# Kernel optimization log

Hardware: AMD Instinct MI355X
Metric: run time of the kernel (lower is better)

## Reference

```python
import jax, jax.numpy as jnp
import numpy as np

INPUT_H = 512
INPUT_W = 512
POOL = 5
BN_EPS = 1e-5


def setup_inputs() -> dict:
    key = jax.random.key(0)
    ks = jax.random.split(key, 8)
    B = 16
    c3 = jax.random.normal(ks[0], (B, 512, 64, 64), jnp.float32)
    c4 = jax.random.normal(ks[1], (B, 1024, 32, 32), jnp.float32)
    xy = jax.random.uniform(ks[2], (B, 10, 4), jnp.float32) * 512.0
    # ensure x1<=x2, y1<=y2 like real detector boxes
    boxes = jnp.concatenate([jnp.minimum(xy[..., :2], xy[..., 2:]),
                             jnp.maximum(xy[..., :2], xy[..., 2:])], axis=-1)
    w_conv = jax.random.normal(ks[3], (512, 1536), jnp.float32) * 0.02  # 1x1 conv kernel
    b_conv = jnp.zeros((512,), jnp.float32)
    bn_gamma = jnp.ones((512,), jnp.float32)
    bn_beta = jnp.zeros((512,), jnp.float32)
    bn_mean = jax.random.normal(ks[4], (512,), jnp.float32) * 0.1
    bn_var = jax.random.uniform(ks[5], (512,), jnp.float32) * 0.5 + 0.5
    return {"c3": c3, "c4": c4, "boxes": boxes, "w_conv": w_conv, "b_conv": b_conv,
            "bn_gamma": bn_gamma, "bn_beta": bn_beta, "bn_mean": bn_mean, "bn_var": bn_var}


def _bin_weights(lo, hi, size, nout):
    """Adaptive-avg-pool bin weights over axis of length `size` for crop [lo,hi).
    Returns [nout, size] row-stochastic matrix (same math as AdaptiveAvgPool1d bins)."""
    length = hi - lo
    k = jnp.arange(nout)
    starts = lo + (k * length) // nout                      # floor(k*L/n)
    ends = lo + ((k + 1) * length + nout - 1) // nout        # ceil((k+1)*L/n)
    idx = jnp.arange(size)
    mask = (idx[None, :] >= starts[:, None]) & (idx[None, :] < ends[:, None])
    return mask.astype(jnp.float32) / (ends - starts)[:, None].astype(jnp.float32)


def reference(c3, c4, boxes, w_conv, b_conv, bn_gamma, bn_beta, bn_mean, bn_var):
    B = c3.shape[0]
    c4u = jax.image.resize(c4, (B, c4.shape[1], c4.shape[2] * 2, c4.shape[3] * 2),
                           method='bilinear')
    fused = jnp.concatenate([c3, c4u], axis=1)               # [B,1536,H,W]
    y = jnp.einsum('bchw,oc->bohw', fused, w_conv) + b_conv[None, :, None, None]
    inv = bn_gamma / jnp.sqrt(bn_var + BN_EPS)               # eval-mode BN
    y = y * inv[None, :, None, None] + (bn_beta - bn_mean * inv)[None, :, None, None]
    attr_blob = jax.nn.relu(y)                               # [B,512,H,W]
    H, W = attr_blob.shape[-2:]
    sx = W / INPUT_W
    sy = H / INPUT_H

    def pool_one(feat, box):  # feat [C,H,W], box [4] -> [C,5,5]
        x1 = jnp.clip(jnp.floor(box[0] * sx), 0, W - 1).astype(jnp.int32)
        y1 = jnp.clip(jnp.floor(box[1] * sy), 0, H - 1).astype(jnp.int32)
        x2 = jnp.clip(jnp.ceil(box[2] * sx), 0, W - 1).astype(jnp.int32)
        y2 = jnp.clip(jnp.ceil(box[3] * sy), 0, H - 1).astype(jnp.int32)
        x2 = jnp.where(x2 <= x1, jnp.minimum(x1 + 1, W), x2)
        y2 = jnp.where(y2 <= y1, jnp.minimum(y1 + 1, H), y2)
        wy = _bin_weights(y1, y2, H, POOL)                   # [5,H]
        wx = _bin_weights(x1, x2, W, POOL)                   # [5,W]
        return jnp.einsum('ph,chw,qw->cpq', wy, feat, wx)

    obj_blob = jax.vmap(lambda f, bx: jax.vmap(lambda b: pool_one(f, b))(bx))(attr_blob, boxes)
    return boxes, obj_blob  # ([B,10,4], [B,10,512,5,5])
```

## Files before the change

### kernel.cpp

```cpp
#include <hip/hip_runtime.h>
#include <stdint.h>

#define FH 64
#define FW 64
#define CIN 1536
#define C3C 512
#define C4C 1024
#define COUT 512
#define BATCH 16
#define NPIX 4096
#define NBOX 10
#define MPAD 256
#define KT128 12

#define NB_FU 12288
#define NB_P  4000
#define NB_W  768
#define NB_BN 2
#define NB_CP 3
#define NB_TOT (NB_FU + NB_P + NB_W + NB_BN + NB_CP)

typedef float v4f __attribute__((ext_vector_type(4)));
typedef long  v2l __attribute__((ext_vector_type(2)));

#define GLOAD_LDS16(g, l) __builtin_amdgcn_global_load_lds( \
    (const __attribute__((address_space(1))) void*)(g),     \
    (__attribute__((address_space(3))) void*)(l), 16, 0, 0)

#define BARRIER() asm volatile("s_barrier" ::: "memory")

__device__ __forceinline__ uint32_t pack4_fp8(float a, float b, float c, float d) {
    int lo = __builtin_amdgcn_cvt_pk_fp8_f32(a, b, 0, false);
    int v  = __builtin_amdgcn_cvt_pk_fp8_f32(c, d, lo, true);
    return (uint32_t)v;
}
__device__ __forceinline__ unsigned char f32_to_fp8(float a) {
    return (unsigned char)(__builtin_amdgcn_cvt_pk_fp8_f32(a, a, 0, false) & 0xff);
}


__global__ __launch_bounds__(256) void mega_pre(
        const float* __restrict__ c3, const float* __restrict__ c4,
        const float* __restrict__ boxes,
        const float* __restrict__ w_conv, const float* __restrict__ b_conv,
        const float* __restrict__ bng, const float* __restrict__ bnb,
        const float* __restrict__ bnm, const float* __restrict__ bnv,
        unsigned char* __restrict__ fusedT, unsigned char* __restrict__ P,
        unsigned char* __restrict__ w8,
        float* __restrict__ scale, float* __restrict__ shift,
        float* __restrict__ out) {
    __shared__ uint32_t lds[64 * 36];
    const int bid = blockIdx.x;
    const int t   = threadIdx.x;

    if (bid < NB_FU) {
        int ct = bid % 12;
        int rest = bid / 12;
        int y  = rest & 63;
        int b  = rest >> 6;
        int pg = t & 15;
        int cq = t >> 4;

        #pragma unroll
        for (int r = 0; r < 2; ++r) {
            int cquad = cq + 16 * r;
            float vv[4][4];
            if (ct < 4) {
                int ch = ct * 128 + 4 * cquad;
                const float* src = c3 + (((size_t)(b * C3C + ch) * FH + y) * FW) + 4 * pg;
                #pragma unroll
                for (int k = 0; k < 4; ++k) {
                    float4 f = *(const float4*)(src + (size_t)k * (FH * FW));
                    vv[k][0] = f.x; vv[k][1] = f.y; vv[k][2] = f.z; vv[k][3] = f.w;
                }
            } else {
                int ch = ct * 128 - 512 + 4 * cquad;
                int jy = y >> 1;
                int jyB = min(max(jy + ((y & 1) ? 1 : -1), 0), 31);
                const float* base = c4 + (size_t)(b * C4C + ch) * 1024;
                #pragma unroll
                for (int k = 0; k < 4; ++k) {
                    const float* pc = base + (size_t)k * 1024;
                    float2 f0 = *(const float2*)(pc + jy * 32 + 2 * pg);
                    float2 f1 = *(const float2*)(pc + jyB * 32 + 2 * pg);
                    float rbA = 0.75f * f0.x + 0.25f * f1.x;
                    float rbB = 0.75f * f0.y + 0.25f * f1.y;
                    float rbm = __shfl_up(rbB, 1, 16);
                    float rbp = __shfl_down(rbA, 1, 16);
                    if (pg == 0)  rbm = rbA;
                    if (pg == 15) rbp = rbB;
                    vv[k][0] = 0.75f * rbA + 0.25f * rbm;
                    vv[k][1] = 0.75f * rbA + 0.25f * rbB;
                    vv[k][2] = 0.75f * rbB + 0.25f * rbA;
                    vv[k][3] = 0.75f * rbB + 0.25f * rbp;
                }
            }
            int wp = ((cquad >> 1) & 3) * 8 + (cquad >> 3) * 2 + (cquad & 1);
            #pragma unroll
            for (int i = 0; i < 4; ++i) {
                int px = 4 * pg + i;
                lds[px * 36 + 4 * ((wp >> 2) ^ ((px >> 1) & 7)) + (wp & 3)] =
                    pack4_fp8(vv[0][i], vv[1][i], vv[2][i], vv[3][i]);
            }
        }
        __syncthreads();
        int g = t & 7;
        #pragma unroll
        for (int rr2 = 0; rr2 < 2; ++rr2) {
            int px = (t >> 3) + 32 * rr2;
            uint4 w = *(const uint4*)(&lds[px * 36 + 4 * (g ^ ((px >> 1) & 7))]);
            *(uint4*)(fusedT + ((size_t)b * NPIX + y * FW + px) * CIN + ct * 128 + g * 16) = w;
        }
    } else if (bid < NB_FU + NB_P) {
        int id  = bid - NB_FU;
        int br  = id % 160;
        int m25 = id / 160;
        int b   = br / NBOX;
        int m   = (br % NBOX) * 25 + m25;
        int p   = m25 / 5, q = m25 % 5;
        int y   = t >> 2;
        int x0  = (t & 3) * 16;
        const float* bx = boxes + (size_t)br * 4;
        int x1 = min(max((int)floorf(bx[0] * 0.125f), 0), 63);
        int y1 = min(max((int)floorf(bx[1] * 0.125f), 0), 63);
        int x2 = min(max((int)ceilf (bx[2] * 0.125f), 0), 63);
        int y2 = min(max((int)ceilf (bx[3] * 0.125f), 0), 63);
        if (x2 <= x1) x2 = min(x1 + 1, 64);
        if (y2 <= y1) y2 = min(y1 + 1, 64);
        int Lx = x2 - x1, Ly = y2 - y1;
        int sx = x1 + (q * Lx) / 5;
        int ex = x1 + ((q + 1) * Lx + 4) / 5;
        int sy = y1 + (p * Ly) / 5;
        int ey = y1 + ((p + 1) * Ly + 4) / 5;
        float wyv  = (y >= sy && y < ey) ? 1.0f / (float)(ey - sy) : 0.0f;
        float pval = 64.0f * wyv / (float)(ex - sx);
        float v[16];
        #pragma unroll
        for (int i = 0; i < 16; ++i) {
            int xi = x0 + i;
            v[i] = (xi >= sx && xi < ex) ? pval : 0.0f;
        }
        uint4 w;
        w.x = pack4_fp8(v[0],  v[1],  v[2],  v[3]);
        w.y = pack4_fp8(v[4],  v[5],  v[6],  v[7]);
        w.z = pack4_fp8(v[8],  v[9],  v[10], v[11]);
        w.w = pack4_fp8(v[12], v[13], v[14], v[15]);
        *(uint4*)(P + ((size_t)b * MPAD + m) * NPIX + y * FW + x0) = w;
    } else if (bid < NB_FU + NB_P + NB_W) {
        int i = (bid - NB_FU - NB_P) * 256 + t;
        if (i < COUT * CIN / 4) {
            float4 f = *(const float4*)(w_conv + i * 4);
            uint32_t v = pack4_fp8(f.x * 16.0f, f.y * 16.0f, f.z * 16.0f, f.w * 16.0f);
            int c0 = (i * 4) % CIN;
            int o  = (i * 4) / CIN;
            int k7 = c0 & 127;
            int pos = ((k7 >> 3) & 3) * 32 + (k7 >> 5) * 8 + (k7 & 7);
            *(uint32_t*)(w8 + (size_t)o * CIN + (c0 & ~127) + pos) = v;
        }
    } else if (bid < NB_FU + NB_P + NB_W + NB_BN) {
        int o = (bid - NB_FU - NB_P - NB_W) * 256 + t;
        if (o < COUT) {
            float inv = bng[o] / sqrtf(bnv[o] + 1e-5f);
            scale[o] = inv * 0.0625f;
            shift[o] = bnb[o] + inv * (b_conv[o] - bnm[o]);
        }
    } else {
        int i = (bid - NB_FU - NB_P - NB_W - NB_BN) * 256 + t;
        if (i < 640) out[i] = boxes[i];
    }
}

__global__ __launch_bounds__(512, 2) void gemm_bn_relu(
        const unsigned char* __restrict__ w8,
        const unsigned char* __restrict__ fusedT,
        const float* __restrict__ scale, const float* __restrict__ shift,
        unsigned char* __restrict__ attr) {
    __shared__ __align__(16) unsigned char lds_a[2][32768];
    __shared__ __align__(16) unsigned char lds_b[2][32768];
    const int t  = threadIdx.x;
    const int n0 = blockIdx.x * 256;
    const int o0 = blockIdx.y * 256;
    const int b  = blockIdx.z;
    const int wave = t >> 6, lane = t & 63;
    const int wm = wave & 1, wn = wave >> 1;
    const int quad = lane >> 4, l16 = lane & 15;
    const int cp0 = (((quad << 1) ^ (l16 & 7)) << 4);
    const int cp1 = cp0 ^ 16;
    const unsigned char* fb = fusedT + (size_t)b * NPIX * CIN;

    const int rr = t >> 3;
    const int cg = (t & 7) ^ (rr & 7);
    const unsigned char* gA = w8 + (size_t)(o0 + rr) * CIN + cg * 16;
    const unsigned char* gB = fb + (size_t)(n0 + rr) * CIN + cg * 16;

#define SA(u, kt, d) GLOAD_LDS16(gA + (size_t)(u) * (64 * CIN) + (kt) * 128, \
                                 &lds_a[d][(u) * 8192 + t * 16])
#define SB(u, kt, d) GLOAD_LDS16(gB + (size_t)(u) * (64 * CIN) + (kt) * 128, \
                                 &lds_b[d][(u) * 8192 + t * 16])
#define RAV(d, ph, i, cp) (*(const v2l*)(&lds_a[d][((wm * 128 + (ph) * 64 + (i) * 16 + l16) << 7) + (cp)]))
#define RBV(d, j, cp)     (*(const v2l*)(&lds_b[d][((wn * 64 + (j) * 16 + l16) << 7) + (cp)]))

    v4f acc[8][4];
    #pragma unroll
    for (int i = 0; i < 8; ++i)
        #pragma unroll
        for (int j = 0; j < 4; ++j) acc[i][j] = (v4f)0.0f;

    SA(0, 0, 0); SA(1, 0, 0); SA(2, 0, 0); SA(3, 0, 0);
    SB(0, 0, 0); SB(1, 0, 0); SB(2, 0, 0); SB(3, 0, 0);
    SA(0, 1, 1); SA(2, 1, 1); SB(0, 1, 1); SB(1, 1, 1); SB(2, 1, 1); SB(3, 1, 1);
    asm volatile("s_waitcnt vmcnt(6)" ::: "memory");
    BARRIER();

    v2l ah0[4], ah1[4], bh0[4], bh1[4];

    for (int kt = 0; kt < KT128; ++kt) {
        const int cur = kt & 1, nxt = cur ^ 1;

        #pragma unroll
        for (int i = 0; i < 4; ++i) { ah0[i] = RAV(cur, 0, i, cp0); ah1[i] = RAV(cur, 0, i, cp1); }
        #pragma unroll
        for (int j = 0; j < 4; ++j) { bh0[j] = RBV(cur, j, cp0); bh1[j] = RBV(cur, j, cp1); }
        if (kt > 0 && kt + 1 < KT128) {
            SA(0, kt + 1, nxt); SA(2, kt + 1, nxt);
            SB(0, kt + 1, nxt); SB(1, kt + 1, nxt);
            SB(2, kt + 1, nxt); SB(3, kt + 1, nxt);
        }
        __builtin_amdgcn_s_setprio(1);
        #pragma unroll
        for (int s = 0; s < 2; ++s)
            #pragma unroll
            for (int i = 0; i < 4; ++i)
                #pragma unroll
                for (int j = 0; j < 4; ++j)
                    acc[i][j] = __builtin_amdgcn_mfma_f32_16x16x32_fp8_fp8(ah0[i][s], bh0[j][s], acc[i][j], 0, 0, 0);
        #pragma unroll
        for (int s = 0; s < 2; ++s)
            #pragma unroll
            for (int i = 0; i < 4; ++i)
                #pragma unroll
                for (int j = 0; j < 4; ++j)
                    acc[i][j] = __builtin_amdgcn_mfma_f32_16x16x32_fp8_fp8(ah1[i][s], bh1[j][s], acc[i][j], 0, 0, 0);
        __builtin_amdgcn_s_setprio(0);
        if (kt + 1 < KT128) { asm volatile("s_waitcnt vmcnt(6)" ::: "memory"); }
        else               { asm volatile("s_waitcnt vmcnt(0)" ::: "memory"); }
        BARRIER();

        #pragma unroll
        for (int i = 0; i < 4; ++i) { ah0[i] = RAV(cur, 1, i, cp0); ah1[i] = RAV(cur, 1, i, cp1); }
        if (kt + 1 < KT128) { SA(1, kt + 1, nxt); SA(3, kt + 1, nxt); }
        __builtin_amdgcn_s_setprio(1);
        #pragma unroll
        for (int s = 0; s < 2; ++s)
            #pragma unroll
            for (int i = 0; i < 4; ++i)
                #pragma unroll
                for (int j = 0; j < 4; ++j)
                    acc[4 + i][j] = __builtin_amdgcn_mfma_f32_16x16x32_fp8_fp8(ah0[i][s], bh0[j][s], acc[4 + i][j], 0, 0, 0);
        #pragma unroll
        for (int s = 0; s < 2; ++s)
            #pragma unroll
            for (int i = 0; i < 4; ++i)
                #pragma unroll
                for (int j = 0; j < 4; ++j)
                    acc[4 + i][j] = __builtin_amdgcn_mfma_f32_16x16x32_fp8_fp8(ah1[i][s], bh1[j][s], acc[4 + i][j], 0, 0, 0);
        __builtin_amdgcn_s_setprio(0);
        if (kt + 1 < KT128) { asm volatile("s_waitcnt vmcnt(2)" ::: "memory"); }
        BARRIER();
    }

    unsigned char* ab = attr + (size_t)b * COUT * NPIX;
    #pragma unroll
    for (int a = 0; a < 8; ++a) {
        int obase = o0 + wm * 128 + (a >> 2) * 64 + (a & 3) * 16 + quad * 4;
        #pragma unroll
        for (int r = 0; r < 4; ++r) {
            int oo = obase + r;
            float sc = scale[oo], sh = shift[oo];
            #pragma unroll
            for (int j = 0; j < 4; ++j) {
                int n = n0 + wn * 64 + j * 16 + l16;
                float v = fmaxf(acc[a][j][r] * sc + sh, 0.0f);
                ab[(size_t)oo * NPIX + n] = f32_to_fp8(v);
            }
        }
    }
#undef SA
#undef SB
#undef RAV
#undef RBV
}

__global__ __launch_bounds__(256) void pool_gemm(
        const unsigned char* __restrict__ P,
        const unsigned char* __restrict__ attr,
        float* __restrict__ part2) {
    __shared__ __align__(16) unsigned char lds_a[128 * 64];
    __shared__ __align__(16) unsigned char lds_b[128 * 64];
    int t  = threadIdx.x;
    int m0 = blockIdx.x * 128;
    int c0 = (blockIdx.y & 3) * 128;
    int seg = blockIdx.y >> 2;
    int b  = blockIdx.z;
    int wave = t >> 6, lane = t & 63;
    int wm = wave & 1, wn = wave >> 1;
    int quad = lane >> 4, l16 = lane & 15;
    const unsigned char* Pb = P + (size_t)b * MPAD * NPIX + seg * 1024;
    const unsigned char* ab = attr + (size_t)b * COUT * NPIX + seg * 1024;

    v4f acc[4][4];
    #pragma unroll
    for (int i = 0; i < 4; ++i)
        #pragma unroll
        for (int j = 0; j < 4; ++j) acc[i][j] = (v4f)0.0f;

    int row = t >> 2;
    int cg  = (t & 3) ^ ((row >> 1) & 3);
    const unsigned char* ga0 = Pb + (size_t)(m0 + row) * NPIX + cg * 16;
    const unsigned char* ga1 = Pb + (size_t)(m0 + row + 64) * NPIX + cg * 16;
    const unsigned char* gb0 = ab + (size_t)(c0 + row) * NPIX + cg * 16;
    const unsigned char* gb1 = ab + (size_t)(c0 + row + 64) * NPIX + cg * 16;
    unsigned char* la0 = lds_a + t * 16;
    unsigned char* la1 = lds_a + 4096 + t * 16;
    unsigned char* lb0 = lds_b + t * 16;
    unsigned char* lb1 = lds_b + 4096 + t * 16;

    int ra[4], rb[4];
    #pragma unroll
    for (int i = 0; i < 4; ++i) { ra[i] = wm * 64 + i * 16 + l16; rb[i] = wn * 64 + i * 16 + l16; }
    int q2 = quad >> 1, q1 = (quad & 1) * 8;

    for (int kt = 0; kt < 1024 / 64; ++kt) {
        __syncthreads();
        GLOAD_LDS16(ga0, la0);
        GLOAD_LDS16(ga1, la1);
        GLOAD_LDS16(gb0, lb0);
        GLOAD_LDS16(gb1, lb1);
        ga0 += 64; ga1 += 64; gb0 += 64; gb1 += 64;
        __syncthreads();

        #pragma unroll
        for (int s = 0; s < 2; ++s) {
            long af[4], bf[4];
            #pragma unroll
            for (int i = 0; i < 4; ++i) {
                int pa = (2 * s + q2) ^ ((ra[i] >> 1) & 3);
                af[i] = *(const long*)(lds_a + ra[i] * 64 + pa * 16 + q1);
                int pb = (2 * s + q2) ^ ((rb[i] >> 1) & 3);
                bf[i] = *(const long*)(lds_b + rb[i] * 64 + pb * 16 + q1);
            }
            #pragma unroll
            for (int i = 0; i < 4; ++i)
                #pragma unroll
                for (int j = 0; j < 4; ++j)
                    acc[i][j] = __builtin_amdgcn_mfma_f32_16x16x32_fp8_fp8(af[i], bf[j], acc[i][j], 0, 0, 0);
        }
    }

    float* pp = part2 + (((size_t)seg * BATCH + b) * MPAD) * COUT;
    #pragma unroll
    for (int i = 0; i < 4; ++i) {
        #pragma unroll
        for (int r = 0; r < 4; ++r) {
            int mrow = m0 + wm * 64 + i * 16 + quad * 4 + r;
            #pragma unroll
            for (int j = 0; j < 4; ++j) {
                int c = c0 + wn * 64 + j * 16 + l16;
                pp[(size_t)mrow * COUT + c] = acc[i][j][r];
            }
        }
    }
}

__global__ __launch_bounds__(256) void pool_reduce(const float* __restrict__ part2,
                                                   float* __restrict__ out) {
    const size_t SEG = (size_t)BATCH * MPAD * COUT;
    int i = blockIdx.x * 256 + threadIdx.x;
    int c = i & (COUT - 1);
    int m = (i >> 9) & (MPAD - 1);
    int b = i >> 17;
    if (m >= 250) return;
    float s = part2[i] + part2[i + SEG] + part2[i + 2 * SEG] + part2[i + 3 * SEG];
    int box = m / 25, bin = m - box * 25;
    out[640 + ((size_t)(b * NBOX + box) * COUT + c) * 25 + bin] = s * 0.015625f;
}

extern "C" void kernel_launch(void* const* d_in, const int* in_sizes, int n_in,
                              void* d_out, int out_size, void* d_ws, size_t ws_size,
                              hipStream_t stream) {
    const float* c3     = (const float*)d_in[0];
    const float* c4     = (const float*)d_in[1];
    const float* boxes  = (const float*)d_in[2];
    const float* w_conv = (const float*)d_in[3];
    const float* b_conv = (const float*)d_in[4];
    const float* bng    = (const float*)d_in[5];
    const float* bnb    = (const float*)d_in[6];
    const float* bnm    = (const float*)d_in[7];
    const float* bnv    = (const float*)d_in[8];
    float* out = (float*)d_out;

    char* ws = (char*)d_ws;
    unsigned char* fusedT = (unsigned char*)ws;
    unsigned char* P      = (unsigned char*)(ws + 100663296);
    float*         part2  = (float*)(ws + 117440512);
    unsigned char* w8     = (unsigned char*)(ws + 150994944);
    float*         scale  = (float*)(ws + 151781376);
    float*         shift  = (float*)(ws + 151783424);
    unsigned char* attr   = (unsigned char*)(ws + 151785472);

    mega_pre<<<NB_TOT, 256, 0, stream>>>(c3, c4, boxes, w_conv, b_conv,
                                         bng, bnb, bnm, bnv,
                                         fusedT, P, w8, scale, shift, out);
    gemm_bn_relu<<<dim3(16, 2, 16), 512, 0, stream>>>(w8, fusedT, scale, shift, attr);
    pool_gemm<<<dim3(2, 16, 16), 256, 0, stream>>>(P, attr, part2);
    pool_reduce<<<(BATCH * MPAD * COUT) / 256, 256, 0, stream>>>(part2, out);
    (void)in_sizes; (void)n_in; (void)out_size; (void)ws_size;
}
```

Measured before the change: 379.5 us.

## Double-buffer pool GEMM with 128-byte K tiles and matching permuted layouts

The pool GEMM moves from a single-buffered 64-byte K tile, with two barriers per step, to a double-buffered 128-byte K tile that prefetches the next stage while MFMAs run, and raises wave priority around the MFMA block. To let each lane read 16-byte fragments, the producers now write P and the attr tensor in a permuted column order within each 128-byte chunk, so the contraction order stays consistent. This should hide global-load latency and halve the number of loop iterations and barriers. The cost is four times the LDS per block, 64 KB, which may lower occupancy, plus scattered byte stores in the conv epilogue.

Measured after the change: 376.9 us. No clear change (-0.7%).

```diff
diff --git a/kernel.cpp b/kernel.cpp
--- a/kernel.cpp
+++ b/kernel.cpp
@@ -145,7 +145,11 @@
         w.y = pack4_fp8(v[4],  v[5],  v[6],  v[7]);
         w.z = pack4_fp8(v[8],  v[9],  v[10], v[11]);
         w.w = pack4_fp8(v[12], v[13], v[14], v[15]);
-        *(uint4*)(P + ((size_t)b * MPAD + m) * NPIX + y * FW + x0) = w;
+        unsigned char* dst = P + ((size_t)b * MPAD + m) * NPIX + (y >> 1) * 128;
+        int g0 = 8 * (y & 1) + 2 * (t & 3);
+        int g1 = g0 + 1;
+        *(uint2*)(dst + (g0 & 3) * 32 + (g0 >> 2) * 8) = make_uint2(w.x, w.y);
+        *(uint2*)(dst + (g1 & 3) * 32 + (g1 >> 2) * 8) = make_uint2(w.z, w.w);
     } else if (bid < NB_FU + NB_P + NB_W) {
         int i = (bid - NB_FU - NB_P) * 256 + t;
         if (i < COUT * CIN / 4) {
@@ -270,6 +274,11 @@
     }
 
     unsigned char* ab = attr + (size_t)b * COUT * NPIX;
+    int nn[4];
+    #pragma unroll
+    for (int j = 0; j < 4; ++j)
+        nn[j] = n0 + (wn >> 1) * 128 + ((2 * j + (l16 >> 3)) & 3) * 32
+              + (2 * (wn & 1) + (j >> 1)) * 8 + (l16 & 7);
     #pragma unroll
     for (int a = 0; a < 8; ++a) {
         int obase = o0 + wm * 128 + (a >> 2) * 64 + (a & 3) * 16 + quad * 4;
@@ -279,9 +288,8 @@
             float sc = scale[oo], sh = shift[oo];
             #pragma unroll
             for (int j = 0; j < 4; ++j) {
-                int n = n0 + wn * 64 + j * 16 + l16;
                 float v = fmaxf(acc[a][j][r] * sc + sh, 0.0f);
-                ab[(size_t)oo * NPIX + n] = f32_to_fp8(v);
+                ab[(size_t)oo * NPIX + nn[j]] = f32_to_fp8(v);
             }
         }
     }
@@ -295,8 +303,8 @@
         const unsigned char* __restrict__ P,
         const unsigned char* __restrict__ attr,
         float* __restrict__ part2) {
-    __shared__ __align__(16) unsigned char lds_a[128 * 64];
-    __shared__ __align__(16) unsigned char lds_b[128 * 64];
+    __shared__ __align__(16) unsigned char lds_a[2][16384];
+    __shared__ __align__(16) unsigned char lds_b[2][16384];
     int t  = threadIdx.x;
     int m0 = blockIdx.x * 128;
     int c0 = (blockIdx.y & 3) * 128;
@@ -305,8 +313,22 @@
     int wave = t >> 6, lane = t & 63;
     int wm = wave & 1, wn = wave >> 1;
     int quad = lane >> 4, l16 = lane & 15;
+    const int cp0 = (((quad << 1) ^ (l16 & 7)) << 4);
+    const int cp1 = cp0 ^ 16;
     const unsigned char* Pb = P + (size_t)b * MPAD * NPIX + seg * 1024;
     const unsigned char* ab = attr + (size_t)b * COUT * NPIX + seg * 1024;
+
+    int rr = t >> 3;
+    int cg = (t & 7) ^ (rr & 7);
+    const unsigned char* gA = Pb + (size_t)(m0 + rr) * NPIX + cg * 16;
+    const unsigned char* gB = ab + (size_t)(c0 + rr) * NPIX + cg * 16;
+
+#define SPA(u, st, d) GLOAD_LDS16(gA + (size_t)(u) * (32 * NPIX) + (st) * 128, \
+                                  &lds_a[d][(u) * 4096 + t * 16])
+#define SPB(u, st, d) GLOAD_LDS16(gB + (size_t)(u) * (32 * NPIX) + (st) * 128, \
+                                  &lds_b[d][(u) * 4096 + t * 16])
+#define PRA(d, i, cp) (*(const v2l*)(&lds_a[d][((wm * 64 + (i) * 16 + l16) << 7) + (cp)]))
+#define PRB(d, j, cp) (*(const v2l*)(&lds_b[d][((wn * 64 + (j) * 16 + l16) << 7) + (cp)]))
 
     v4f acc[4][4];
     #pragma unroll
@@ -314,47 +336,40 @@
         #pragma unroll
         for (int j = 0; j < 4; ++j) acc[i][j] = (v4f)0.0f;
 
-    int row = t >> 2;
-    int cg  = (t & 3) ^ ((row >> 1) & 3);
-    const unsigned char* ga0 = Pb + (size_t)(m0 + row) * NPIX + cg * 16;
-    const unsigned char* ga1 = Pb + (size_t)(m0 + row + 64) * NPIX + cg * 16;
-    const unsigned char* gb0 = ab + (size_t)(c0 + row) * NPIX + cg * 16;
-    const unsigned char* gb1 = ab + (size_t)(c0 + row + 64) * NPIX + cg * 16;
-    unsigned char* la0 = lds_a + t * 16;
-    unsigned char* la1 = lds_a + 4096 + t * 16;
-    unsigned char* lb0 = lds_b + t * 16;
-    unsigned char* lb1 = lds_b + 4096 + t * 16;
-
-    int ra[4], rb[4];
-    #pragma unroll
-    for (int i = 0; i < 4; ++i) { ra[i] = wm * 64 + i * 16 + l16; rb[i] = wn * 64 + i * 16 + l16; }
-    int q2 = quad >> 1, q1 = (quad & 1) * 8;
-
-    for (int kt = 0; kt < 1024 / 64; ++kt) {
-        __syncthreads();
-        GLOAD_LDS16(ga0, la0);
-        GLOAD_LDS16(ga1, la1);
-        GLOAD_LDS16(gb0, lb0);
-        GLOAD_LDS16(gb1, lb1);
-        ga0 += 64; ga1 += 64; gb0 += 64; gb1 += 64;
-        __syncthreads();
-
-        #pragma unroll
-        for (int s = 0; s < 2; ++s) {
-            long af[4], bf[4];
-            #pragma unroll
-            for (int i = 0; i < 4; ++i) {
-                int pa = (2 * s + q2) ^ ((ra[i] >> 1) & 3);
-                af[i] = *(const long*)(lds_a + ra[i] * 64 + pa * 16 + q1);
-                int pb = (2 * s + q2) ^ ((rb[i] >> 1) & 3);
-                bf[i] = *(const long*)(lds_b + rb[i] * 64 + pb * 16 + q1);
-            }
-            #pragma unroll
-            for (int i = 0; i < 4; ++i)
-                #pragma unroll
-                for (int j = 0; j < 4; ++j)
-                    acc[i][j] = __builtin_amdgcn_mfma_f32_16x16x32_fp8_fp8(af[i], bf[j], acc[i][j], 0, 0, 0);
-        }
+    SPA(0, 0, 0); SPA(1, 0, 0); SPA(2, 0, 0); SPA(3, 0, 0);
+    SPB(0, 0, 0); SPB(1, 0, 0); SPB(2, 0, 0); SPB(3, 0, 0);
+    asm volatile("s_waitcnt vmcnt(0)" ::: "memory");
+    BARRIER();
+
+    for (int k = 0; k < 8; ++k) {
+        const int cur = k & 1, nxt = cur ^ 1;
+        v2l a0[4], a1[4], b0[4], b1[4];
+        #pragma unroll
+        for (int i = 0; i < 4; ++i) { a0[i] = PRA(cur, i, cp0); a1[i] = PRA(cur, i, cp1); }
+        #pragma unroll
+        for (int j = 0; j < 4; ++j) { b0[j] = PRB(cur, j, cp0); b1[j] = PRB(cur, j, cp1); }
+        if (k + 1 < 8) {
+            SPA(0, k + 1, nxt); SPA(1, k + 1, nxt); SPA(2, k + 1, nxt); SPA(3, k + 1, nxt);
+            SPB(0, k + 1, nxt); SPB(1, k + 1, nxt); SPB(2, k + 1, nxt); SPB(3, k + 1, nxt);
+        }
+        __builtin_amdgcn_s_setprio(1);
+        #pragma unroll
+        for (int s = 0; s < 2; ++s)
+            #pragma unroll
+            for (int i = 0; i < 4; ++i)
+                #pragma unroll
+                for (int j = 0; j < 4; ++j)
+                    acc[i][j] = __builtin_amdgcn_mfma_f32_16x16x32_fp8_fp8(a0[i][s], b0[j][s], acc[i][j], 0, 0, 0);
+        #pragma unroll
+        for (int s = 0; s < 2; ++s)
+            #pragma unroll
+            for (int i = 0; i < 4; ++i)
+                #pragma unroll
+                for (int j = 0; j < 4; ++j)
+                    acc[i][j] = __builtin_amdgcn_mfma_f32_16x16x32_fp8_fp8(a1[i][s], b1[j][s], acc[i][j], 0, 0, 0);
+        __builtin_amdgcn_s_setprio(0);
+        asm volatile("s_waitcnt vmcnt(0)" ::: "memory");
+        BARRIER();
     }
 
     float* pp = part2 + (((size_t)seg * BATCH + b) * MPAD) * COUT;
@@ -370,6 +385,10 @@
             }
         }
     }
+#undef SPA
+#undef SPB
+#undef PRA
+#undef PRB
 }
 
 __global__ __launch_bounds__(256) void pool_reduce(const float* __restrict__ part2,
```
